# Performance work log

Measured on AMD Instinct MI355X. Metric: run time of the kernel, lower is better.

Reference implementation:

```python
import jax, jax.numpy as jnp
import numpy as np
import math

B, S, D_MODEL = 2, 2048, 1024
NUM_HEADS, D_KEY, D_VALUE = 16, 64, 64


def setup_inputs() -> dict:
    key = jax.random.key(0)
    ks = jax.random.split(key, 7)
    query = jax.random.normal(ks[0], (B, S, D_MODEL), dtype=jnp.float32)
    k_in = jax.random.normal(ks[1], (B, S, D_MODEL), dtype=jnp.float32)
    v_in = jax.random.normal(ks[2], (B, S, D_MODEL), dtype=jnp.float32)
    # boolean mask, True = masked out (masked_fill_ semantics); causal mask
    mask = jnp.triu(jnp.ones((S, S), dtype=bool), k=1)[None, None, :, :]
    scale = 1.0 / math.sqrt(D_MODEL)
    w_q = jax.random.normal(ks[3], (D_MODEL, NUM_HEADS * D_KEY), dtype=jnp.float32) * scale
    w_k = jax.random.normal(ks[4], (D_MODEL, NUM_HEADS * D_KEY), dtype=jnp.float32) * scale
    w_v = jax.random.normal(ks[5], (D_MODEL, NUM_HEADS * D_VALUE), dtype=jnp.float32) * scale
    w_o = jax.random.normal(ks[6], (NUM_HEADS * D_VALUE, D_MODEL), dtype=jnp.float32) * scale
    return {"query": query, "key": k_in, "value": v_in, "mask": mask,
            "w_q": w_q, "w_k": w_k, "w_v": w_v, "w_o": w_o}


def reference(query, key, value, mask, w_q, w_k, w_v, w_o):
    b, sq, _ = query.shape
    sk = key.shape[1]
    # projections, split heads: [B, H, S, d]
    q = (query @ w_q).reshape(b, sq, NUM_HEADS, D_KEY).transpose(0, 2, 1, 3)
    k = (key @ w_k).reshape(b, sk, NUM_HEADS, D_KEY).transpose(0, 2, 1, 3)
    v = (value @ w_v).reshape(b, sk, NUM_HEADS, D_VALUE).transpose(0, 2, 1, 3)
    # scaled scores [B, H, Sq, Sk], eager masked softmax (as in source)
    scores = jnp.einsum('bhqd,bhkd->bhqk', q, k) / math.sqrt(D_KEY)
    scores = jnp.where(mask, -jnp.inf, scores)
    attn = jax.nn.softmax(scores, axis=-1)
    # AV, merge heads, output projection (dropout is identity in eval / p=0)
    out = jnp.einsum('bhqk,bhkd->bhqd', attn, v)
    out = out.transpose(0, 2, 1, 3).reshape(b, sq, NUM_HEADS * D_VALUE)
    return out @ w_o
```

## Files before the change

kernel.cpp:

```cpp
#include <hip/hip_runtime.h>


typedef __attribute__((ext_vector_type(8))) short v8s;
typedef __attribute__((ext_vector_type(4))) float v4f;

#define MFMA16(a, b, c) __builtin_amdgcn_mfma_f32_16x16x32_bf16(a, b, c, 0, 0, 0)

#define GLOBAL_AS __attribute__((address_space(1)))
#define LDS_AS __attribute__((address_space(3)))

__device__ __forceinline__ void gload_lds16(const void* g, void* l) {
  __builtin_amdgcn_global_load_lds((const GLOBAL_AS void*)g, (LDS_AS void*)l, 16, 0, 0);
}

__device__ __forceinline__ short f2bf(float f) {
  union { float f; unsigned u; } x; x.f = f;
  unsigned r = x.u + 0x7fffu + ((x.u >> 16) & 1u);
  return (short)(r >> 16);
}

__device__ __forceinline__ unsigned cvtpk_bf16(float a, float b) {
  unsigned r;
  asm("v_cvt_pk_bf16_f32 %0, %1, %2" : "=v"(r) : "v"(a), "v"(b));
  return r;
}

__device__ __forceinline__ float exp2_hw(float x) {
  float r;
  asm("v_exp_f32 %0, %1" : "=v"(r) : "v"(x));
  return r;
}

__global__ __launch_bounds__(256) void wtrans_kernel(const float* __restrict__ w0,
                                                     const float* __restrict__ w1,
                                                     const float* __restrict__ w2,
                                                     const float* __restrict__ w3,
                                                     short* __restrict__ wtbase) {
  __shared__ __align__(16) short tile[64 * 72];
  const int NN = 1024;
  int z = blockIdx.z;
  const float* W = (z == 0) ? w0 : (z == 1) ? w1 : (z == 2) ? w2 : w3;
  short* Wt = wtbase + ((z < 3) ? ((size_t)(z + 1) << 20) : 0);
  float scale = (z == 0) ? 0.125f * 1.44269504f : 1.0f;
  int n0 = blockIdx.x * 64, k0 = blockIdx.y * 64;
  int t = threadIdx.x;
  int r = t >> 4;
  int c4 = (t & 15) * 4;
  for (int rr = r; rr < 64; rr += 16) {
    float4 f = *(const float4*)(W + (size_t)(k0 + rr) * NN + n0 + c4);
    tile[(c4 + 0) * 72 + rr] = f2bf(f.x * scale);
    tile[(c4 + 1) * 72 + rr] = f2bf(f.y * scale);
    tile[(c4 + 2) * 72 + rr] = f2bf(f.z * scale);
    tile[(c4 + 3) * 72 + rr] = f2bf(f.w * scale);
  }
  __syncthreads();
  int nr = t >> 2, kc = (t & 3) * 16;
  v8s v0 = *(const v8s*)&tile[nr * 72 + kc];
  v8s v1 = *(const v8s*)&tile[nr * 72 + kc + 8];
  *(v8s*)(Wt + (size_t)(n0 + nr) * NN + k0 + kc) = v0;
  *(v8s*)(Wt + (size_t)(n0 + nr) * NN + k0 + kc + 8) = v1;
}

__global__ __launch_bounds__(256) void cast3_kernel(const float* __restrict__ s0,
                                                    const float* __restrict__ s1,
                                                    const float* __restrict__ s2,
                                                    short* __restrict__ dst,
                                                    size_t zstride) {
  int z = blockIdx.z;
  const float* src = (z == 0) ? s0 : (z == 1) ? s1 : s2;
  short* d = dst + (size_t)z * zstride;
  int i = (blockIdx.x * 256 + threadIdx.x) * 8;
  float4 f0 = *(const float4*)(src + i);
  float4 f1 = *(const float4*)(src + i + 4);
  v8s v;
  v[0] = f2bf(f0.x); v[1] = f2bf(f0.y); v[2] = f2bf(f0.z); v[3] = f2bf(f0.w);
  v[4] = f2bf(f1.x); v[5] = f2bf(f1.y); v[6] = f2bf(f1.z); v[7] = f2bf(f1.w);
  *(v8s*)(d + i) = v;
}

__global__ __launch_bounds__(256) void vtrans_kernel(const short* __restrict__ Vb,
                                                     short* __restrict__ Vtg) {
  __shared__ __align__(16) short T[64 * 72];
  const int S = 2048, DM = 1024;
  int s0 = blockIdx.x * 64;
  int bh = blockIdx.y;
  int b = bh >> 4, h = bh & 15;
  int t = threadIdx.x;
  int srow = t >> 2, sc = (t & 3) * 16;
  const short* src = Vb + (size_t)(b * S + s0 + srow) * DM + h * 64 + sc;
  v8s a = *(const v8s*)src;
  v8s c = *(const v8s*)(src + 8);
#pragma unroll
  for (int j = 0; j < 8; ++j) {
    int jj = (j + srow) & 7;
    T[(sc + jj) * 72 + srow] = a[jj];
  }
#pragma unroll
  for (int j = 0; j < 8; ++j) {
    int jj = (j + srow) & 7;
    T[(sc + 8 + jj) * 72 + srow] = c[jj];
  }
  __syncthreads();
  int dr = t >> 2, oc = (t & 3) * 16;
  short* dst = Vtg + (size_t)bh * 64 * S + (size_t)dr * S + s0 + oc;
  *(v8s*)dst = *(const v8s*)&T[dr * 72 + oc];
  *(v8s*)(dst + 8) = *(const v8s*)&T[dr * 72 + oc + 8];
}

template <bool OUT_F32>
__global__ __launch_bounds__(256) void gemm97_kernel(
    const short* __restrict__ Ab, size_t sA,
    const short* __restrict__ Btb, size_t sB,
    short* __restrict__ Cb, float* __restrict__ Cf, size_t sC,
    int M, int N, int K) {
  __shared__ __align__(16) short As[2][128 * 32];
  __shared__ __align__(16) short Bs[2][128 * 32];

  int gx = gridDim.x, gy = gridDim.y;
  int id = blockIdx.x + gx * (blockIdx.y + gy * blockIdx.z);
  int nwg = gx * gy * gridDim.z;
  int v = (id & 7) * (nwg >> 3) + (id >> 3);
  int bx = v % gx;
  int by = (v / gx) % gy;
  int bz = v / (gx * gy);

  const short* A = Ab + (size_t)bz * sA;
  const short* Bt = Btb + (size_t)bz * sB;
  int row0 = by * 128, col0 = bx * 128;
  int t = threadIdx.x, lane = t & 63, w = t >> 6;
  int wm = (w >> 1) * 64, wn = (w & 1) * 64;
  int lr = lane & 15, lg = lane >> 4;

  v4f acc[4][4];
#pragma unroll
  for (int i = 0; i < 4; ++i)
#pragma unroll
    for (int j = 0; j < 4; ++j) acc[i][j] = {0.f, 0.f, 0.f, 0.f};

  int rl = lane >> 2, sl = lane & 3;
  int scol = ((sl ^ (rl ^ (rl >> 2))) & 3) * 8;
  const short* gA = A + (size_t)(row0 + w * 16 + rl) * K + scol;
  const short* gB = Bt + (size_t)(col0 + w * 16 + rl) * K + scol;
  const size_t rstep = (size_t)64 * K;

#define GEMM_STAGE(buf, k0_)                              \
  do {                                                    \
    gload_lds16(gA + (k0_), &As[buf][w * 512]);           \
    gload_lds16(gA + rstep + (k0_), &As[buf][(w + 4) * 512]); \
    gload_lds16(gB + (k0_), &Bs[buf][w * 512]);           \
    gload_lds16(gB + rstep + (k0_), &Bs[buf][(w + 4) * 512]); \
  } while (0)

  GEMM_STAGE(0, 0);
  __syncthreads();
  int cur = 0;
  int rsw = (lr ^ (lr >> 2)) & 3;
  for (int k0 = 0; k0 < K; k0 += 32) {
    if (k0 + 32 < K) GEMM_STAGE(cur ^ 1, k0 + 32);
    v8s af[4], bg[4];
#pragma unroll
    for (int mf = 0; mf < 4; ++mf)
      af[mf] = *(const v8s*)&As[cur][(wm + mf * 16 + lr) * 32 + ((lg ^ rsw) * 8)];
#pragma unroll
    for (int nf = 0; nf < 4; ++nf)
      bg[nf] = *(const v8s*)&Bs[cur][(wn + nf * 16 + lr) * 32 + ((lg ^ rsw) * 8)];
    __builtin_amdgcn_s_setprio(1);
#pragma unroll
    for (int mf = 0; mf < 4; ++mf)
#pragma unroll
      for (int nf = 0; nf < 4; ++nf)
        acc[mf][nf] = MFMA16(af[mf], bg[nf], acc[mf][nf]);
    __builtin_amdgcn_s_setprio(0);
    __syncthreads();
    cur ^= 1;
  }
#undef GEMM_STAGE

#pragma unroll
  for (int mf = 0; mf < 4; ++mf)
#pragma unroll
    for (int nf = 0; nf < 4; ++nf)
#pragma unroll
      for (int r = 0; r < 4; ++r) {
        int row = row0 + wm + mf * 16 + lg * 4 + r;
        int col = col0 + wn + nf * 16 + lr;
        if (OUT_F32)
          (Cf + (size_t)bz * sC)[(size_t)row * N + col] = acc[mf][nf][r];
        else
          (Cb + (size_t)bz * sC)[(size_t)row * N + col] = f2bf(acc[mf][nf][r]);
      }
}

__global__ __launch_bounds__(512, 4) void attn_kernel(const short* __restrict__ Qm,
                                                      const short* __restrict__ Km,
                                                      const short* __restrict__ Vt_g,
                                                      short* __restrict__ Cm) {
  const int S = 2048, DM = 1024;
  __shared__ __align__(16) short lds[21504];
  short* Ks0 = lds;
  short* Vs0 = lds + 8192;
  short* Pt = lds + 16384;
  v4f* scr = (v4f*)lds;

  int id = blockIdx.y * 16 + blockIdx.x;
  int v = (id & 7) * 64 + (id >> 3);
  int bh = v >> 4;
  int px = v & 15;
  int b = bh >> 4, h = bh & 15;
  int t = threadIdx.x, lane = t & 63, w = t >> 6;
  int g = w & 3, hh = w >> 2;
  int lr = lane & 15, lg = lane >> 4;
  size_t base = (size_t)b * S * DM + h * 64;
  size_t vbase = (size_t)bh * 64 * S;

  int srow = w * 8 + (lane >> 3);
  int scol = ((lane & 7) ^ (lane >> 3)) * 8;
  const short* gK = Km + base + (size_t)srow * DM + scol;
  const short* gV = Vt_g + vbase + (size_t)srow * S + scol;
  int sw = (lr & 7) * 8;

  const v8s vone = {0x3F80, 0x3F80, 0x3F80, 0x3F80,
                    0x3F80, 0x3F80, 0x3F80, 0x3F80};

#define ATTN_STAGE(buf, kt_)                                                  \
  do {                                                                        \
    size_t k0_ = (size_t)(kt_) * 64;                                          \
    gload_lds16(gK + k0_ * DM, &Ks0[(buf) * 4096 + w * 512]);                 \
    gload_lds16(gV + k0_, &Vs0[(buf) * 4096 + w * 512]);                      \
  } while (0)

  short* Cp = Cm + base;

#pragma unroll 1
  for (int qsel = 0; qsel < 2; ++qsel) {
    int qt = qsel ? px : (31 - px);
    int qbase = qt * 64 + g * 16;
    int qg = qbase + lr;
    int nkt = qt + 1;

    const short* Qp = Qm + base + (size_t)(qbase + lr) * DM + lg * 8;
    v8s q0 = *(const v8s*)Qp;
    v8s q1 = *(const v8s*)(Qp + 32);

    v4f o[5];
#pragma unroll
    for (int d4 = 0; d4 < 5; ++d4) o[d4] = {0.f, 0.f, 0.f, 0.f};

    ATTN_STAGE(0, 0);
    __syncthreads();
    int cur = 0;
#pragma unroll 1
    for (int kt = 0; kt < nkt; ++kt) {
      if (kt + 1 < nkt) ATTN_STAGE(cur ^ 1, kt + 1);
      int k0 = kt * 64;
      const short* Kc = &Ks0[cur * 4096];
      const short* Vc = &Vs0[cur * 4096];

      v8s ka0[2], ka1[2], vf[4];
#pragma unroll
      for (int t2 = 0; t2 < 2; ++t2) {
        int kr = hh * 32 + t2 * 16 + lr;
        ka0[t2] = *(const v8s*)&Kc[kr * 64 + ((lg * 8) ^ sw)];
        ka1[t2] = *(const v8s*)&Kc[kr * 64 + ((32 + lg * 8) ^ sw)];
      }
#pragma unroll
      for (int d4 = 0; d4 < 4; ++d4)
        vf[d4] = *(const v8s*)&Vc[(d4 * 16 + lr) * 64 + ((hh * 32 + lg * 8) ^ sw)];

      v4f st[2];
      __builtin_amdgcn_s_setprio(1);
#pragma unroll
      for (int t2 = 0; t2 < 2; ++t2) {
        v4f s = {0.f, 0.f, 0.f, 0.f};
        s = MFMA16(ka0[t2], q0, s);
        s = MFMA16(ka1[t2], q1, s);
        st[t2] = s;
      }
      __builtin_amdgcn_s_setprio(0);

      if (kt == nkt - 1) {
#pragma unroll
        for (int t2 = 0; t2 < 2; ++t2)
#pragma unroll
          for (int r = 0; r < 4; ++r)
            if (k0 + hh * 32 + t2 * 16 + lg * 4 + r > qg) st[t2][r] = -1e30f;
      }

#pragma unroll
      for (int t2 = 0; t2 < 2; ++t2) {
        uint2 u;
        u.x = cvtpk_bf16(exp2_hw(st[t2][0]), exp2_hw(st[t2][1]));
        u.y = cvtpk_bf16(exp2_hw(st[t2][2]), exp2_hw(st[t2][3]));
        *(uint2*)&Pt[w * 640 + lr * 40 + t2 * 16 + lg * 4] = u;
      }
      v8s pa = *(const v8s*)&Pt[w * 640 + lr * 40 + lg * 8];

      __builtin_amdgcn_s_setprio(1);
#pragma unroll
      for (int d4 = 0; d4 < 4; ++d4) o[d4] = MFMA16(pa, vf[d4], o[d4]);
      o[4] = MFMA16(pa, vone, o[4]);
      __builtin_amdgcn_s_setprio(0);
      __syncthreads();
      cur ^= 1;
    }

    if (hh == 1) {
#pragma unroll
      for (int d4 = 0; d4 < 5; ++d4) scr[(g * 5 + d4) * 64 + lane] = o[d4];
    }
    __syncthreads();
    if (hh == 0) {
#pragma unroll
      for (int d4 = 0; d4 < 5; ++d4) {
        v4f p = scr[(g * 5 + d4) * 64 + lane];
#pragma unroll
        for (int r = 0; r < 4; ++r) o[d4][r] += p[r];
      }
      float sv[4];
#pragma unroll
      for (int r = 0; r < 4; ++r) sv[r] = 1.0f / o[4][r];
#pragma unroll
      for (int r = 0; r < 4; ++r)
#pragma unroll
        for (int d4 = 0; d4 < 4; ++d4)
          Cp[(size_t)(qbase + lg * 4 + r) * DM + d4 * 16 + lr] =
              f2bf(o[d4][r] * sv[r]);
    }
    __syncthreads();
  }
#undef ATTN_STAGE
}

extern "C" void kernel_launch(void* const* d_in, const int* in_sizes, int n_in,
                              void* d_out, int out_size, void* d_ws, size_t ws_size,
                              hipStream_t stream) {
  const float* q_in = (const float*)d_in[0];
  const float* k_in = (const float*)d_in[1];
  const float* v_in = (const float*)d_in[2];
  const float* w_q = (const float*)d_in[4];
  const float* w_k = (const float*)d_in[5];
  const float* w_v = (const float*)d_in[6];
  const float* w_o = (const float*)d_in[7];
  float* outp = (float*)d_out;

  short* ws = (short*)d_ws;
  const size_t M1 = (size_t)1 << 20;
  short* Wto = ws;
  short* Wtq = ws + 1 * M1;
  dim3 tb(256);
  dim3 tba(512);

  wtrans_kernel<<<dim3(16, 16, 4), tb, 0, stream>>>(w_q, w_k, w_v, w_o, ws);

  bool big = ws_size >= ((size_t)56 << 20);
  if (big) {
    short* X = ws + 4 * M1;
    short* Qb = ws + 16 * M1;
    short* Vb = ws + 24 * M1;
    short* Vtg = ws + 4 * M1;
    short* Cb = ws + 8 * M1;
    cast3_kernel<<<dim3(2048, 1, 3), tb, 0, stream>>>(q_in, k_in, v_in, X, 4 * M1);
    gemm97_kernel<false><<<dim3(8, 32, 3), tb, 0, stream>>>(
        X, 4 * M1, Wtq, M1, Qb, nullptr, 4 * M1, 4096, 1024, 1024);
    vtrans_kernel<<<dim3(32, 32), tb, 0, stream>>>(Vb, Vtg);
    attn_kernel<<<dim3(16, 32), tba, 0, stream>>>(Qb, ws + 20 * M1, Vtg, Cb);
    gemm97_kernel<true><<<dim3(8, 32, 1), tb, 0, stream>>>(
        Cb, 0, Wto, 0, nullptr, outp, 0, 4096, 1024, 1024);
  } else {
    short* X = ws + 4 * M1;
    short* Qb = ws + 8 * M1;
    short* Kb = ws + 12 * M1;
    short* Vb = ws + 16 * M1;
    short* Vtg = ws + 1 * M1;
    short* Cb = Vb;
    cast3_kernel<<<dim3(2048, 1, 1), tb, 0, stream>>>(q_in, q_in, q_in, X, 0);
    gemm97_kernel<false><<<dim3(8, 32, 1), tb, 0, stream>>>(
        X, 0, Wtq, 0, Qb, nullptr, 0, 4096, 1024, 1024);
    cast3_kernel<<<dim3(2048, 1, 1), tb, 0, stream>>>(k_in, k_in, k_in, X, 0);
    gemm97_kernel<false><<<dim3(8, 32, 1), tb, 0, stream>>>(
        X, 0, Wtq + M1, 0, Kb, nullptr, 0, 4096, 1024, 1024);
    cast3_kernel<<<dim3(2048, 1, 1), tb, 0, stream>>>(v_in, v_in, v_in, X, 0);
    gemm97_kernel<false><<<dim3(8, 32, 1), tb, 0, stream>>>(
        X, 0, Wtq + 2 * M1, 0, Vb, nullptr, 0, 4096, 1024, 1024);
    vtrans_kernel<<<dim3(32, 32), tb, 0, stream>>>(Vb, Vtg);
    attn_kernel<<<dim3(16, 32), tba, 0, stream>>>(Qb, Kb, Vtg, Cb);
    gemm97_kernel<true><<<dim3(8, 32, 1), tb, 0, stream>>>(
        Cb, 0, Wto, 0, nullptr, outp, 0, 4096, 1024, 1024);
  }
}
```

Before: 118.7 us.

## Fuse fp32-to-bf16 input cast into projection GEMM and widen K tile

```diff
diff --git a/kernel.cpp b/kernel.cpp
--- a/kernel.cpp
+++ b/kernel.cpp
@@ -61,23 +61,6 @@
   *(v8s*)(Wt + (size_t)(n0 + nr) * NN + k0 + kc + 8) = v1;
 }
 
-__global__ __launch_bounds__(256) void cast3_kernel(const float* __restrict__ s0,
-                                                    const float* __restrict__ s1,
-                                                    const float* __restrict__ s2,
-                                                    short* __restrict__ dst,
-                                                    size_t zstride) {
-  int z = blockIdx.z;
-  const float* src = (z == 0) ? s0 : (z == 1) ? s1 : s2;
-  short* d = dst + (size_t)z * zstride;
-  int i = (blockIdx.x * 256 + threadIdx.x) * 8;
-  float4 f0 = *(const float4*)(src + i);
-  float4 f1 = *(const float4*)(src + i + 4);
-  v8s v;
-  v[0] = f2bf(f0.x); v[1] = f2bf(f0.y); v[2] = f2bf(f0.z); v[3] = f2bf(f0.w);
-  v[4] = f2bf(f1.x); v[5] = f2bf(f1.y); v[6] = f2bf(f1.z); v[7] = f2bf(f1.w);
-  *(v8s*)(d + i) = v;
-}
-
 __global__ __launch_bounds__(256) void vtrans_kernel(const short* __restrict__ Vb,
                                                      short* __restrict__ Vtg) {
   __shared__ __align__(16) short T[64 * 72];
@@ -107,14 +90,16 @@
   *(v8s*)(dst + 8) = *(const v8s*)&T[dr * 72 + oc + 8];
 }
 
-template <bool OUT_F32>
-__global__ __launch_bounds__(256) void gemm97_kernel(
+template <bool A_F32, bool OUT_F32>
+__global__ __launch_bounds__(256) void gemm2_kernel(
+    const float* __restrict__ a0, const float* __restrict__ a1,
+    const float* __restrict__ a2,
     const short* __restrict__ Ab, size_t sA,
     const short* __restrict__ Btb, size_t sB,
     short* __restrict__ Cb, float* __restrict__ Cf, size_t sC,
     int M, int N, int K) {
-  __shared__ __align__(16) short As[2][128 * 32];
-  __shared__ __align__(16) short Bs[2][128 * 32];
+  __shared__ __align__(16) short As[2][128 * 64];
+  __shared__ __align__(16) short Bs[2][128 * 64];
 
   int gx = gridDim.x, gy = gridDim.y;
   int id = blockIdx.x + gx * (blockIdx.y + gy * blockIdx.z);
@@ -124,7 +109,6 @@
   int by = (v / gx) % gy;
   int bz = v / (gx * gy);
 
-  const short* A = Ab + (size_t)bz * sA;
   const short* Bt = Btb + (size_t)bz * sB;
   int row0 = by * 128, col0 = bx * 128;
   int t = threadIdx.x, lane = t & 63, w = t >> 6;
@@ -137,44 +121,91 @@
 #pragma unroll
     for (int j = 0; j < 4; ++j) acc[i][j] = {0.f, 0.f, 0.f, 0.f};
 
-  int rl = lane >> 2, sl = lane & 3;
-  int scol = ((sl ^ (rl ^ (rl >> 2))) & 3) * 8;
-  const short* gA = A + (size_t)(row0 + w * 16 + rl) * K + scol;
-  const short* gB = Bt + (size_t)(col0 + w * 16 + rl) * K + scol;
-  const size_t rstep = (size_t)64 * K;
-
-#define GEMM_STAGE(buf, k0_)                              \
-  do {                                                    \
-    gload_lds16(gA + (k0_), &As[buf][w * 512]);           \
-    gload_lds16(gA + rstep + (k0_), &As[buf][(w + 4) * 512]); \
-    gload_lds16(gB + (k0_), &Bs[buf][w * 512]);           \
-    gload_lds16(gB + rstep + (k0_), &Bs[buf][(w + 4) * 512]); \
-  } while (0)
-
-  GEMM_STAGE(0, 0);
+  int crow = lane >> 3;
+  int scol = ((lane & 7) ^ crow) * 8;
+  const short* gB = Bt + (size_t)(col0 + crow) * K + scol;
+  const short* gA_s =
+      A_F32 ? nullptr : (Ab + (size_t)bz * sA + (size_t)(row0 + crow) * K + scol);
+
+  int ar = t >> 1, ak = (t & 1) * 32;
+  const float* gA_f = nullptr;
+  if (A_F32) {
+    const float* Af = (bz == 0) ? a0 : (bz == 1) ? a1 : a2;
+    gA_f = Af + (size_t)(row0 + ar) * K + ak;
+  }
+  float4 fa[8];
+
+#define STAGE_B(buf, k0_)                                                   \
+  {                                                                         \
+    _Pragma("unroll") for (int c4 = 0; c4 < 4; ++c4) {                      \
+      int c = w + c4 * 4;                                                   \
+      gload_lds16(gB + (size_t)(c * 8) * K + (k0_), &Bs[buf][c * 512]);     \
+    }                                                                       \
+  }
+#define STAGE_A_DMA(buf, k0_)                                               \
+  {                                                                         \
+    _Pragma("unroll") for (int c4 = 0; c4 < 4; ++c4) {                      \
+      int c = w + c4 * 4;                                                   \
+      gload_lds16(gA_s + (size_t)(c * 8) * K + (k0_), &As[buf][c * 512]);   \
+    }                                                                       \
+  }
+#define STAGE_A_LOAD(k0_)                                                   \
+  {                                                                         \
+    _Pragma("unroll") for (int j = 0; j < 8; ++j)                           \
+        fa[j] = *(const float4*)(gA_f + (k0_) + j * 4);                     \
+  }
+#define STAGE_A_WRITE(buf)                                                  \
+  {                                                                         \
+    _Pragma("unroll") for (int j = 0; j < 4; ++j) {                         \
+      uint4 pk;                                                             \
+      pk.x = cvtpk_bf16(fa[2 * j].x, fa[2 * j].y);                          \
+      pk.y = cvtpk_bf16(fa[2 * j].z, fa[2 * j].w);                          \
+      pk.z = cvtpk_bf16(fa[2 * j + 1].x, fa[2 * j + 1].y);                  \
+      pk.w = cvtpk_bf16(fa[2 * j + 1].z, fa[2 * j + 1].w);                  \
+      *(uint4*)&As[buf][ar * 64 + ((((t & 1) * 4 + j) ^ (ar & 7)) * 8)] = pk; \
+    }                                                                       \
+  }
+
+  if (A_F32) STAGE_A_LOAD(0);
+  STAGE_B(0, 0);
+  if (A_F32) { STAGE_A_WRITE(0); } else { STAGE_A_DMA(0, 0); }
   __syncthreads();
+
   int cur = 0;
-  int rsw = (lr ^ (lr >> 2)) & 3;
-  for (int k0 = 0; k0 < K; k0 += 32) {
-    if (k0 + 32 < K) GEMM_STAGE(cur ^ 1, k0 + 32);
-    v8s af[4], bg[4];
-#pragma unroll
-    for (int mf = 0; mf < 4; ++mf)
-      af[mf] = *(const v8s*)&As[cur][(wm + mf * 16 + lr) * 32 + ((lg ^ rsw) * 8)];
-#pragma unroll
-    for (int nf = 0; nf < 4; ++nf)
-      bg[nf] = *(const v8s*)&Bs[cur][(wn + nf * 16 + lr) * 32 + ((lg ^ rsw) * 8)];
-    __builtin_amdgcn_s_setprio(1);
-#pragma unroll
-    for (int mf = 0; mf < 4; ++mf)
+  for (int k0 = 0; k0 < K; k0 += 64) {
+    bool next = (k0 + 64 < K);
+    if (next) {
+      if (A_F32) STAGE_A_LOAD(k0 + 64);
+      STAGE_B(cur ^ 1, k0 + 64);
+      if (!A_F32) STAGE_A_DMA(cur ^ 1, k0 + 64);
+    }
+#pragma unroll
+    for (int kk = 0; kk < 2; ++kk) {
+      v8s af[4], bg[4];
+#pragma unroll
+      for (int mf = 0; mf < 4; ++mf)
+        af[mf] = *(const v8s*)&As[cur][(wm + mf * 16 + lr) * 64 +
+                                       (((kk * 4 + lg) ^ (lr & 7)) * 8)];
 #pragma unroll
       for (int nf = 0; nf < 4; ++nf)
-        acc[mf][nf] = MFMA16(af[mf], bg[nf], acc[mf][nf]);
-    __builtin_amdgcn_s_setprio(0);
+        bg[nf] = *(const v8s*)&Bs[cur][(wn + nf * 16 + lr) * 64 +
+                                       (((kk * 4 + lg) ^ (lr & 7)) * 8)];
+      __builtin_amdgcn_s_setprio(1);
+#pragma unroll
+      for (int mf = 0; mf < 4; ++mf)
+#pragma unroll
+        for (int nf = 0; nf < 4; ++nf)
+          acc[mf][nf] = MFMA16(af[mf], bg[nf], acc[mf][nf]);
+      __builtin_amdgcn_s_setprio(0);
+    }
+    if (next && A_F32) STAGE_A_WRITE(cur ^ 1);
     __syncthreads();
     cur ^= 1;
   }
-#undef GEMM_STAGE
+#undef STAGE_B
+#undef STAGE_A_DMA
+#undef STAGE_A_LOAD
+#undef STAGE_A_WRITE
 
 #pragma unroll
   for (int mf = 0; mf < 4; ++mf)
@@ -347,44 +378,21 @@
   const size_t M1 = (size_t)1 << 20;
   short* Wto = ws;
   short* Wtq = ws + 1 * M1;
+  short* Qb = ws + 4 * M1;
+  short* Kb = ws + 8 * M1;
+  short* Vb = ws + 12 * M1;
+  short* Vtg = ws + 16 * M1;
+  short* Cb = Vb;
   dim3 tb(256);
   dim3 tba(512);
 
   wtrans_kernel<<<dim3(16, 16, 4), tb, 0, stream>>>(w_q, w_k, w_v, w_o, ws);
-
-  bool big = ws_size >= ((size_t)56 << 20);
-  if (big) {
-    short* X = ws + 4 * M1;
-    short* Qb = ws + 16 * M1;
-    short* Vb = ws + 24 * M1;
-    short* Vtg = ws + 4 * M1;
-    short* Cb = ws + 8 * M1;
-    cast3_kernel<<<dim3(2048, 1, 3), tb, 0, stream>>>(q_in, k_in, v_in, X, 4 * M1);
-    gemm97_kernel<false><<<dim3(8, 32, 3), tb, 0, stream>>>(
-        X, 4 * M1, Wtq, M1, Qb, nullptr, 4 * M1, 4096, 1024, 1024);
-    vtrans_kernel<<<dim3(32, 32), tb, 0, stream>>>(Vb, Vtg);
-    attn_kernel<<<dim3(16, 32), tba, 0, stream>>>(Qb, ws + 20 * M1, Vtg, Cb);
-    gemm97_kernel<true><<<dim3(8, 32, 1), tb, 0, stream>>>(
-        Cb, 0, Wto, 0, nullptr, outp, 0, 4096, 1024, 1024);
-  } else {
-    short* X = ws + 4 * M1;
-    short* Qb = ws + 8 * M1;
-    short* Kb = ws + 12 * M1;
-    short* Vb = ws + 16 * M1;
-    short* Vtg = ws + 1 * M1;
-    short* Cb = Vb;
-    cast3_kernel<<<dim3(2048, 1, 1), tb, 0, stream>>>(q_in, q_in, q_in, X, 0);
-    gemm97_kernel<false><<<dim3(8, 32, 1), tb, 0, stream>>>(
-        X, 0, Wtq, 0, Qb, nullptr, 0, 4096, 1024, 1024);
-    cast3_kernel<<<dim3(2048, 1, 1), tb, 0, stream>>>(k_in, k_in, k_in, X, 0);
-    gemm97_kernel<false><<<dim3(8, 32, 1), tb, 0, stream>>>(
-        X, 0, Wtq + M1, 0, Kb, nullptr, 0, 4096, 1024, 1024);
-    cast3_kernel<<<dim3(2048, 1, 1), tb, 0, stream>>>(v_in, v_in, v_in, X, 0);
-    gemm97_kernel<false><<<dim3(8, 32, 1), tb, 0, stream>>>(
-        X, 0, Wtq + 2 * M1, 0, Vb, nullptr, 0, 4096, 1024, 1024);
-    vtrans_kernel<<<dim3(32, 32), tb, 0, stream>>>(Vb, Vtg);
-    attn_kernel<<<dim3(16, 32), tba, 0, stream>>>(Qb, Kb, Vtg, Cb);
-    gemm97_kernel<true><<<dim3(8, 32, 1), tb, 0, stream>>>(
-        Cb, 0, Wto, 0, nullptr, outp, 0, 4096, 1024, 1024);
-  }
-}
+  gemm2_kernel<true, false><<<dim3(8, 32, 3), tb, 0, stream>>>(
+      q_in, k_in, v_in, nullptr, 0, Wtq, M1, Qb, nullptr, 4 * M1,
+      4096, 1024, 1024);
+  vtrans_kernel<<<dim3(32, 32), tb, 0, stream>>>(Vb, Vtg);
+  attn_kernel<<<dim3(16, 32), tba, 0, stream>>>(Qb, Kb, Vtg, Cb);
+  gemm2_kernel<false, true><<<dim3(8, 32, 1), tb, 0, stream>>>(
+      nullptr, nullptr, nullptr, Cb, 0, Wto, 0, nullptr, outp, 0,
+      4096, 1024, 1024);
+}
```

Measured after the change: 135.3 us. +14.0%, slower.
